# Kernel optimization log

Hardware: AMD Instinct MI355X
Metric: run time of the kernel (lower is better)

Reference implementation:

```python
import jax, jax.numpy as jnp
import numpy as np

L = 48.0      # cubic box edge
DL = 4.0      # k-grid spacing param -> nk = int(L/DL) = 12
N = 8192      # atoms
D = 128       # feature channels
TWOPI = 2.0 * np.pi


def _k_index_sets():
    """Replicates torch mask.nonzero() ordering and the (k_vectors - 1) index
    shift of compute_potential_optimized. The shifted indices are remapped to
    effective integer exponents (torch negative indexing wraps, i.e. modulo)."""
    nk = int(L / DL)
    kx = np.arange(nk + 1)
    ky = np.arange(-nk, nk + 1)
    kz = np.arange(-nk, nk + 1)
    KX, KY, KZ = np.meshgrid(kx, ky, kz, indexing='ij')
    ksq = KX.astype(np.float64) ** 2 + KY ** 2 + KZ ** 2
    mask = (ksq <= (L / DL) ** 2) & (ksq > 0)
    ix, iy, iz = np.nonzero(mask)  # row-major, same order as torch .nonzero()
    # forward potential: value[:, :, ix-1, iy-1, iz-1] with wraparound ->
    # effective exponents via modulo of the per-axis table sizes
    ex = (ix - 1) % (nk + 1)                      # eikx col c -> exponent c
    ey = ((iy - 1) % (2 * nk + 1)) - nk           # eiky col c -> exponent c-nk
    ez = ((iz - 1) % (2 * nk + 1)) - nk
    k_fwd = np.stack([ex, ey, ez], axis=1).astype(np.int32)
    # inverse transform: unshifted valid k-vectors, negative sign in exponent
    k_inv = np.stack([ix, iy - nk, iz - nk], axis=1).astype(np.int32)
    return k_fwd, k_inv


def setup_inputs() -> dict:
    key = jax.random.key(0)
    kq, kk, kv, kr = jax.random.split(key, 4)
    k_fwd, k_inv = _k_index_sets()
    cell = jnp.eye(3, dtype=jnp.float32)[None] * jnp.float32(L)  # [1,3,3]
    return {
        'q_vector': jax.random.normal(kq, (N, D), dtype=jnp.float32),
        'k_vector': jax.random.normal(kk, (N, D), dtype=jnp.float32),
        'v_vector': jax.random.normal(kv, (N, D), dtype=jnp.float32),
        'positions': jax.random.uniform(kr, (N, 3), dtype=jnp.float32) * jnp.float32(L),
        'cell': cell,
        'batch': jnp.zeros((N,), dtype=jnp.int64),
        'k_fwd': jnp.asarray(k_fwd),
        'k_inv': jnp.asarray(k_inv),
    }


def reference(q_vector, k_vector, v_vector, positions, cell, batch, k_fwd, k_inv):
    # single batch (batch is all zeros); box = diagonal of the cell
    box = jnp.diagonal(cell.reshape(-1, 3, 3), axis1=-2, axis2=-1)[0]  # [3]
    rfrac = positions / box                                            # [n,3]
    # plane waves at the selected k-vectors; |eik| == 1
    phase_f = TWOPI * (rfrac @ k_fwd.T.astype(rfrac.dtype))            # [n,K]
    eik_f = jnp.exp(1j * phase_f)                                      # complex64
    phase_i = TWOPI * (rfrac @ k_inv.T.astype(rfrac.dtype))
    eik_i = jnp.exp(-1j * phase_i)                                     # [n,K]
    cdt = eik_f.dtype
    # k/v potentials: structure-factor sums over atoms -> [K,d]
    k_pot = jnp.einsum('nk,nd->kd', eik_f, k_vector.astype(cdt))
    v_pot = jnp.einsum('nk,nd->kd', eik_f, v_vector.astype(cdt))
    # |q_pot[n,d,k]| = |q[n,d]|*|eik[n,k]| = |q[n,d]| exactly, so the einsum
    # 'ijk,jk->ij' over abs values collapses to a real GEMM:
    aw = jnp.abs(q_vector) @ jnp.abs(k_pot).T                          # [n,K]
    # max-shift + log_softmax + exp == softmax over the k axis
    sm = jax.nn.softmax(aw, axis=-1)
    # inverse transform fused: sum_k sm[n,k]*eik_i[n,k]*v_pot[k,d]
    out = jnp.real(jnp.einsum('nk,kd->nd', sm.astype(cdt) * eik_i, v_pot))
    return out
```

## Files before the change

### kernel.cpp

```cpp
#include <hip/hip_runtime.h>
#include <hip/hip_bf16.h>

#define D128 128
#define NSPLIT 4
#define KT 32
#define SNR 32
#define SKT 128
#define TOPS 8
#define FCAP 16

typedef float4 f4;
typedef __attribute__((ext_vector_type(8))) short short8v;
typedef __attribute__((ext_vector_type(4))) float f32x4;

__device__ __forceinline__ unsigned short f2bu(float x){
  __hip_bfloat16 h = __float2bfloat16(x);
  return *(unsigned short*)&h;
}
__device__ __forceinline__ float bu2f(unsigned short u){
  return __uint_as_float(((unsigned)u) << 16);
}

#define GLDS16(gp, lp) __builtin_amdgcn_global_load_lds( \
    (const __attribute__((address_space(1))) unsigned int*)(const void*)(gp), \
    (__attribute__((address_space(3))) unsigned int*)(lp), 16, 0, 0)

__global__ __launch_bounds__(256) void k_prep(const float* __restrict__ pos,
    const float* __restrict__ cell, float* __restrict__ rfrac, int N){
  int i = blockIdx.x*256 + threadIdx.x;
  if(i >= N) return;
  float bx = cell[0], by = cell[4], bz = cell[8];
  f4 r; r.x = pos[i*3+0]/bx; r.y = pos[i*3+1]/by; r.z = pos[i*3+2]/bz; r.w = 0.f;
  ((f4*)rfrac)[i] = r;
}

__global__ __launch_bounds__(256) void k_zero(float* __restrict__ p, int total){
  int i = blockIdx.x*256 + threadIdx.x;
  int stride = gridDim.x*256;
  for(; i < total; i += stride) p[i] = 0.f;
}

__global__ __launch_bounds__(256) void k_cvt(const float* __restrict__ q,
    const float* __restrict__ kvec, const float* __restrict__ vvec,
    unsigned short* __restrict__ kvhT, unsigned short* __restrict__ kvlT,
    unsigned short* __restrict__ vvhT, unsigned short* __restrict__ qa_bf, int N){
  __shared__ float sk[32][132], sv[32][132];
  const int tid = threadIdx.x;
  const int c0 = blockIdx.x*32;
  #pragma unroll
  for(int i=0;i<2;i++){
    int idx = tid + i*256;
    int row = idx >> 4, c = idx & 15;
    const float* src = q + (size_t)(c0+row)*D128 + c*8;
    f4 v0 = *(const f4*)src, v1 = *(const f4*)(src+4);
    uint4 o;
    o.x = (unsigned)f2bu(fabsf(v0.x)) | ((unsigned)f2bu(fabsf(v0.y))<<16);
    o.y = (unsigned)f2bu(fabsf(v0.z)) | ((unsigned)f2bu(fabsf(v0.w))<<16);
    o.z = (unsigned)f2bu(fabsf(v1.x)) | ((unsigned)f2bu(fabsf(v1.y))<<16);
    o.w = (unsigned)f2bu(fabsf(v1.z)) | ((unsigned)f2bu(fabsf(v1.w))<<16);
    *(uint4*)(qa_bf + (size_t)(c0+row)*D128 + ((c ^ (row&7))<<3)) = o;
  }
  #pragma unroll
  for(int i=0;i<4;i++){
    int idx = tid + i*256;
    int a = idx >> 5, fq = idx & 31;
    f4 v = ((const f4*)(kvec + (size_t)(c0+a)*D128))[fq];
    *(f4*)&sk[a][fq*4] = v;
    f4 u = ((const f4*)(vvec + (size_t)(c0+a)*D128))[fq];
    *(f4*)&sv[a][fq*4] = u;
  }
  __syncthreads();
  #pragma unroll
  for(int i=0;i<4;i++){
    int idx = tid + i*256;
    int d = idx >> 3, aq = idx & 7;
    size_t ob = (size_t)d*N + c0 + aq*4;
    ushort4 h, l, vh;
    float x0 = sk[aq*4+0][d], x1 = sk[aq*4+1][d], x2 = sk[aq*4+2][d], x3 = sk[aq*4+3][d];
    h.x = f2bu(x0); h.y = f2bu(x1); h.z = f2bu(x2); h.w = f2bu(x3);
    l.x = f2bu(x0 - bu2f(h.x)); l.y = f2bu(x1 - bu2f(h.y));
    l.z = f2bu(x2 - bu2f(h.z)); l.w = f2bu(x3 - bu2f(h.w));
    vh.x = f2bu(sv[aq*4+0][d]); vh.y = f2bu(sv[aq*4+1][d]);
    vh.z = f2bu(sv[aq*4+2][d]); vh.w = f2bu(sv[aq*4+3][d]);
    *(ushort4*)(kvhT + ob) = h;
    *(ushort4*)(kvlT + ob) = l;
    *(ushort4*)(vvhT + ob) = vh;
  }
}

__global__ __launch_bounds__(512) void k_pot_mfma(
    const unsigned short* __restrict__ kvhT, const unsigned short* __restrict__ kvlT,
    const unsigned short* __restrict__ vvhT, const float* __restrict__ rfrac,
    const int* __restrict__ kfwd, float* __restrict__ pot4, int N, int K){
  const int tid = threadIdx.x;
  const int k0 = blockIdx.x*KT;
  const int split = blockIdx.y;
  const int part = N/NSPLIT;
  const int abase = split*part;
  __shared__ unsigned short Ae[2][4][KT][32];
  __shared__ unsigned short Bl[2][3][D128][32];
  const int w = tid >> 6, l = tid & 63, l15 = l & 15, g = l >> 4;
  const int a = tid & 31, rq = tid >> 5;
  float kfr[2][3];
  {
    int r0 = min(k0 + rq*2,     K-1);
    int r1 = min(k0 + rq*2 + 1, K-1);
    kfr[0][0] = (float)kfwd[3*r0]; kfr[0][1] = (float)kfwd[3*r0+1]; kfr[0][2] = (float)kfwd[3*r0+2];
    kfr[1][0] = (float)kfwd[3*r1]; kfr[1][1] = (float)kfwd[3*r1+1]; kfr[1][2] = (float)kfwd[3*r1+2];
  }
  f32x4 acc[2][4];
  #pragma unroll
  for(int i=0;i<2;i++)
    #pragma unroll
    for(int j=0;j<4;j++)
      acc[i][j] = (f32x4){0.f,0.f,0.f,0.f};
  const int rowS = w*16 + (l >> 2);
  const int csrc = (((l & 3) ^ ((l >> 3) & 3)))*8;
  const int cA   = (g ^ ((l15 >> 1) & 3))*8;

  auto stage = [&](int buf, int c0a){
    size_t goff = (size_t)rowS*N + c0a + csrc;
    GLDS16(kvhT + goff, &Bl[buf][0][w*16][0]);
    GLDS16(kvlT + goff, &Bl[buf][1][w*16][0]);
    GLDS16(vvhT + goff, &Bl[buf][2][w*16][0]);
  };
  auto egen = [&](int buf, int c0a){
    f4 rf = ((const f4*)rfrac)[c0a + a];
    #pragma unroll
    for(int rr=0; rr<2; rr++){
      int r = rq*2 + rr;
      float t = rf.x*kfr[rr][0] + rf.y*kfr[rr][1] + rf.z*kfr[rr][2];
      t -= floorf(t);
      float cv = cospif(2.0f*t), sv = sinpif(2.0f*t);
      unsigned short chb = f2bu(cv);
      unsigned short clb = f2bu(cv - bu2f(chb));
      unsigned short shb = f2bu(sv);
      unsigned short slb = f2bu(sv - bu2f(shb));
      int cp = (((a>>3) ^ ((r>>1)&3)) << 3) | (a & 7);
      Ae[buf][0][r][cp] = chb; Ae[buf][1][r][cp] = clb;
      Ae[buf][2][r][cp] = shb; Ae[buf][3][r][cp] = slb;
    }
  };

  stage(0, abase); egen(0, abase);
  __syncthreads();
  const int nch = part/32;
  for(int ch=0; ch<nch; ch++){
    int cur = ch & 1;
    if(ch+1 < nch){ stage(cur^1, abase + (ch+1)*32); egen(cur^1, abase + (ch+1)*32); }
    short8v eA[2][4];
    #pragma unroll
    for(int ks=0; ks<2; ks++)
      #pragma unroll
      for(int ar=0; ar<4; ar++)
        eA[ks][ar] = *(const short8v*)&Ae[cur][ar][ks*16 + l15][cA];
    short8v bKh = *(const short8v*)&Bl[cur][0][w*16 + l15][cA];
    short8v bKl = *(const short8v*)&Bl[cur][1][w*16 + l15][cA];
    short8v bVh = *(const short8v*)&Bl[cur][2][w*16 + l15][cA];
    #pragma unroll
    for(int ks=0; ks<2; ks++){
      acc[ks][0] = __builtin_amdgcn_mfma_f32_16x16x32_bf16(eA[ks][0], bKh, acc[ks][0], 0,0,0);
      acc[ks][1] = __builtin_amdgcn_mfma_f32_16x16x32_bf16(eA[ks][2], bKh, acc[ks][1], 0,0,0);
      acc[ks][2] = __builtin_amdgcn_mfma_f32_16x16x32_bf16(eA[ks][0], bVh, acc[ks][2], 0,0,0);
      acc[ks][3] = __builtin_amdgcn_mfma_f32_16x16x32_bf16(eA[ks][2], bVh, acc[ks][3], 0,0,0);
      acc[ks][0] = __builtin_amdgcn_mfma_f32_16x16x32_bf16(eA[ks][0], bKl, acc[ks][0], 0,0,0);
      acc[ks][1] = __builtin_amdgcn_mfma_f32_16x16x32_bf16(eA[ks][2], bKl, acc[ks][1], 0,0,0);
      acc[ks][0] = __builtin_amdgcn_mfma_f32_16x16x32_bf16(eA[ks][1], bKh, acc[ks][0], 0,0,0);
      acc[ks][1] = __builtin_amdgcn_mfma_f32_16x16x32_bf16(eA[ks][3], bKh, acc[ks][1], 0,0,0);
    }
    __syncthreads();
  }
  size_t M = (size_t)K*D128;
  #pragma unroll
  for(int ks=0; ks<2; ks++){
    #pragma unroll
    for(int reg=0; reg<4; reg++){
      int k = k0 + ks*16 + g*4 + reg;
      if(k < K){
        int d = w*16 + l15;
        size_t base = (size_t)k*D128 + d;
        atomicAdd(&pot4[base],       acc[ks][0][reg]);
        atomicAdd(&pot4[base + M],   acc[ks][1][reg]);
        atomicAdd(&pot4[base + 2*M], acc[ks][2][reg]);
        atomicAdd(&pot4[base + 3*M], acc[ks][3][reg]);
      }
    }
  }
}

__global__ __launch_bounds__(256) void k_merge(const float* __restrict__ pot4,
    float* __restrict__ kabs, unsigned short* __restrict__ kabs_swz,
    float* __restrict__ vcm, float* __restrict__ vsm, int K, int KPAD){
  size_t M = (size_t)K*D128;
  size_t idx = (size_t)blockIdx.x*256 + threadIdx.x;
  if(idx >= (size_t)KPAD*D128) return;
  int k = (int)(idx >> 7), d = (int)(idx & 127);
  size_t sw = (size_t)k*D128 + ((((d>>3) ^ (k&7))<<3) | (d&7));
  if(idx < M){
    float kc = pot4[idx], ks_ = pot4[M+idx], vc = pot4[2*M+idx], vs = pot4[3*M+idx];
    float ab = sqrtf(fmaf(kc,kc, ks_*ks_));
    kabs[idx] = ab;
    vcm[idx] = vc; vsm[idx] = vs;
    kabs_swz[sw] = f2bu(ab);
  } else {
    kabs_swz[sw] = 0;
  }
}

__global__ __launch_bounds__(256) void k_screen(
    const unsigned short* __restrict__ qa_bf, const unsigned short* __restrict__ kabs_swz,
    int* __restrict__ tk, float* __restrict__ taw, int N, int K, int NT){
  const int tid = threadIdx.x;
  const int w = tid >> 6, l = tid & 63, l15 = l & 15, g = l >> 4;
  const int n0 = blockIdx.x*SNR;
  const int ty = blockIdx.y;
  const int k0 = ty*SKT;
  __shared__ unsigned short Kb[SKT][D128];
  __shared__ unsigned short Qa[SNR][D128];
  __shared__ int cnt[SNR];
  __shared__ unsigned mx[SNR];
  if(tid < SNR){ cnt[tid] = 0; mx[tid] = 0u; }
  {
    int row = tid >> 3, s = tid & 7;
    size_t o = ((size_t)(n0+row)*NT + ty)*TOPS + s;
    taw[o] = -1e30f; tk[o] = -1;
  }
  #pragma unroll
  for(int j=0;j<8;j++){
    int sbase = w*512 + j*64;
    GLDS16(kabs_swz + (size_t)k0*D128 + (size_t)(sbase + l)*8,
           ((unsigned short*)Kb) + (size_t)sbase*8);
  }
  #pragma unroll
  for(int j=0;j<2;j++){
    int sbase = w*128 + j*64;
    GLDS16(qa_bf + (size_t)n0*D128 + (size_t)(sbase + l)*8,
           ((unsigned short*)Qa) + (size_t)sbase*8);
  }
  __syncthreads();
  f32x4 acc[2][2];
  #pragma unroll
  for(int i=0;i<2;i++)
    #pragma unroll
    for(int j=0;j<2;j++)
      acc[i][j] = (f32x4){0.f,0.f,0.f,0.f};
  const int sz = l15 & 7;
  #pragma unroll
  for(int ds=0; ds<4; ds++){
    int c = (((ds*4 + g) ^ sz))*8;
    short8v a0 = *(const short8v*)&Kb[w*32 + l15][c];
    short8v a1 = *(const short8v*)&Kb[w*32 + 16 + l15][c];
    short8v b0 = *(const short8v*)&Qa[l15][c];
    short8v b1 = *(const short8v*)&Qa[16 + l15][c];
    acc[0][0] = __builtin_amdgcn_mfma_f32_16x16x32_bf16(a0, b0, acc[0][0], 0,0,0);
    acc[0][1] = __builtin_amdgcn_mfma_f32_16x16x32_bf16(a0, b1, acc[0][1], 0,0,0);
    acc[1][0] = __builtin_amdgcn_mfma_f32_16x16x32_bf16(a1, b0, acc[1][0], 0,0,0);
    acc[1][1] = __builtin_amdgcn_mfma_f32_16x16x32_bf16(a1, b1, acc[1][1], 0,0,0);
  }
  #pragma unroll
  for(int jn=0; jn<2; jn++){
    float m4 = 0.f;
    #pragma unroll
    for(int ks=0; ks<2; ks++)
      #pragma unroll
      for(int r=0; r<4; r++)
        m4 = fmaxf(m4, acc[ks][jn][r]);
    atomicMax(&mx[jn*16 + l15], __float_as_uint(m4));
  }
  __syncthreads();
  #pragma unroll
  for(int jn=0; jn<2; jn++){
    int n = jn*16 + l15;
    float thr = __uint_as_float(mx[n]) - 21.0f;
    #pragma unroll
    for(int ks=0; ks<2; ks++){
      #pragma unroll
      for(int r=0; r<4; r++){
        int k = k0 + w*32 + ks*16 + g*4 + r;
        float aw = acc[ks][jn][r];
        if(k < K && aw >= thr){
          int s = atomicAdd(&cnt[n], 1);
          if(s < TOPS){
            size_t o = ((size_t)(n0+n)*NT + ty)*TOPS + s;
            taw[o] = aw; tk[o] = k;
          }
        }
      }
    }
  }
}

__global__ __launch_bounds__(256) void k_final(const float* __restrict__ q,
    const float* __restrict__ kabs, const float* __restrict__ vcm,
    const float* __restrict__ vsm, const float* __restrict__ rfrac,
    const int* __restrict__ kinv, const int* __restrict__ tk,
    const float* __restrict__ taw, float* __restrict__ out, int N, int K, int NT){
  const int rb = threadIdx.x >> 2;
  const int j  = threadIdx.x & 3;
  const int row = blockIdx.x*64 + rb;
  if(row >= N) return;
  const int NE = NT*TOPS;
  const float* trow = taw + (size_t)row*NE;
  const int*   krow = tk  + (size_t)row*NE;
  float m = -1e30f;
  for(int i=j; i<NE; i+=4) m = fmaxf(m, trow[i]);
  m = fmaxf(m, __shfl_xor(m,1)); m = fmaxf(m, __shfl_xor(m,2));
  __shared__ int lk[64][FCAP];
  __shared__ int lcnt[64];
  if(j==0) lcnt[rb] = 0;
  __syncthreads();
  for(int i=j; i<NE; i+=4){
    float aw = trow[i];
    if(aw >= m - 24.0f){
      int s = atomicAdd(&lcnt[rb], 1);
      if(s < FCAP) lk[rb][s] = krow[i];
    }
  }
  __syncthreads();
  int cn = min(lcnt[rb], FCAP);
  const float* qrow = q + (size_t)row*D128;
  float paw[FCAP];
  for(int e=0; e<cn; e++){
    int k = lk[rb][e];
    const float* ar = kabs + (size_t)k*D128;
    float p = 0.f;
    #pragma unroll
    for(int d=0; d<32; d+=4){
      int dd = j*32 + d;
      f4 qv = *(const f4*)(qrow+dd); f4 av = *(const f4*)(ar+dd);
      p = fmaf(fabsf(qv.x), av.x, p); p = fmaf(fabsf(qv.y), av.y, p);
      p = fmaf(fabsf(qv.z), av.z, p); p = fmaf(fabsf(qv.w), av.w, p);
    }
    p += __shfl_xor(p,1); p += __shfl_xor(p,2);
    paw[e] = p;
  }
  float m2 = -1e30f;
  for(int e=0;e<cn;e++) m2 = fmaxf(m2, paw[e]);
  float w[FCAP]; float Z = 0.f;
  for(int e=0;e<cn;e++){ w[e] = expf(paw[e]-m2); Z += w[e]; }
  float o[32];
  #pragma unroll
  for(int t=0;t<32;t++) o[t]=0.f;
  f4 rf = *(const f4*)(rfrac + (size_t)row*4);
  for(int e=0;e<cn;e++){
    float wn = w[e]/Z;
    if(wn < 1e-7f) continue;
    int k = lk[rb][e];
    float t = rf.x*(float)kinv[k*3] + rf.y*(float)kinv[k*3+1] + rf.z*(float)kinv[k*3+2];
    t -= floorf(t);
    float si = sinpif(2.0f*t), ci = cospif(2.0f*t);
    float wc = wn*ci, wsn = wn*si;
    const float* vcr = vcm + (size_t)k*D128 + j*32;
    const float* vsr = vsm + (size_t)k*D128 + j*32;
    #pragma unroll
    for(int d=0; d<32; d+=4){
      f4 a2 = *(const f4*)(vcr+d); f4 b2 = *(const f4*)(vsr+d);
      o[d]   = fmaf(wc, a2.x, fmaf(wsn, b2.x, o[d]));
      o[d+1] = fmaf(wc, a2.y, fmaf(wsn, b2.y, o[d+1]));
      o[d+2] = fmaf(wc, a2.z, fmaf(wsn, b2.z, o[d+2]));
      o[d+3] = fmaf(wc, a2.w, fmaf(wsn, b2.w, o[d+3]));
    }
  }
  float* orow = out + (size_t)row*D128 + j*32;
  #pragma unroll
  for(int d=0; d<32; d+=4)
    *(f4*)(orow+d) = make_float4(o[d], o[d+1], o[d+2], o[d+3]);
}

extern "C" void kernel_launch(void* const* d_in, const int* in_sizes, int n_in,
                              void* d_out, int out_size, void* d_ws, size_t ws_size,
                              hipStream_t stream){
  const float* q    = (const float*)d_in[0];
  const float* kvec = (const float*)d_in[1];
  const float* vvec = (const float*)d_in[2];
  const float* pos  = (const float*)d_in[3];
  const float* cell = (const float*)d_in[4];
  const int*   kfwd = (const int*)d_in[6];
  const int*   kinv = (const int*)d_in[7];
  const int N = in_sizes[3]/3;
  const int K = in_sizes[6]/3;
  const int NT = (K + SKT - 1)/SKT;
  const int KPAD = NT*SKT;
  const int KTILES = (K + KT - 1)/KT;

  float* ws = (float*)d_ws;
  size_t o = 0;
  float* rfrac    = ws + o; o += (size_t)N*4;
  float* pot4     = ws + o; o += (size_t)4*K*D128;
  float* kabs     = ws + o; o += (size_t)K*D128;
  float* vcm      = ws + o; o += (size_t)K*D128;
  float* vsm      = ws + o; o += (size_t)K*D128;
  unsigned short* kabs_swz = (unsigned short*)(ws + o); o += (size_t)KPAD*D128/2 + 4;
  unsigned short* qa_bf    = (unsigned short*)(ws + o); o += (size_t)N*D128/2 + 4;
  float* taw      = ws + o; o += (size_t)N*NT*TOPS;
  int*   tk       = (int*)(ws + o); o += (size_t)N*NT*TOPS;
  unsigned short* kvhT = (unsigned short*)(ws + o); o += (size_t)D128*N/2;
  unsigned short* kvlT = (unsigned short*)(ws + o); o += (size_t)D128*N/2;
  unsigned short* vvhT = (unsigned short*)(ws + o); o += (size_t)D128*N/2;
  float* out = (float*)d_out;

  k_prep<<<dim3((N+255)/256), dim3(256), 0, stream>>>(pos, cell, rfrac, N);
  k_zero<<<dim3(1024), dim3(256), 0, stream>>>(pot4, 4*K*D128);
  k_cvt<<<dim3(N/32), dim3(256), 0, stream>>>(q, kvec, vvec, kvhT, kvlT, vvhT, qa_bf, N);
  k_pot_mfma<<<dim3(KTILES, NSPLIT), dim3(512), 0, stream>>>(
      kvhT, kvlT, vvhT, rfrac, kfwd, pot4, N, K);
  k_merge<<<dim3((KPAD*D128 + 255)/256), dim3(256), 0, stream>>>(
      pot4, kabs, kabs_swz, vcm, vsm, K, KPAD);
  k_screen<<<dim3(N/SNR, NT), dim3(256), 0, stream>>>(qa_bf, kabs_swz, tk, taw, N, K, NT);
  k_final<<<dim3((N+63)/64), dim3(256), 0, stream>>>(
      q, kabs, vcm, vsm, rfrac, kinv, tk, taw, out, N, K, NT);
}
```

Baseline: 271.8 us.

## Retile potential MFMA kernel, fuse prep into convert, use hardware sin/cos

The potential kernel now covers 64 k-vectors per block instead of 32 and splits atoms eight ways instead of four. Each thread generates plane-wave values for two atoms and two k-vectors, writing packed 32-bit bf16 pairs to LDS, so each staged B tile is reused across more k rows. The separate position-normalisation kernel is folded into the convert kernel, removing one launch. The sincospi calls are replaced by the hardware fract, sin and cos intrinsics in both the generation and final kernels. That trades accuracy for speed and uses more accumulator registers, which could lower occupancy.

```diff
diff --git a/kernel.cpp b/kernel.cpp
--- a/kernel.cpp
+++ b/kernel.cpp
@@ -2,8 +2,8 @@
 #include <hip/hip_bf16.h>
 
 #define D128 128
-#define NSPLIT 4
-#define KT 32
+#define NSPLIT 8
+#define KT 64
 #define SNR 32
 #define SKT 128
 #define TOPS 8
@@ -25,28 +25,27 @@
     (const __attribute__((address_space(1))) unsigned int*)(const void*)(gp), \
     (__attribute__((address_space(3))) unsigned int*)(lp), 16, 0, 0)
 
-__global__ __launch_bounds__(256) void k_prep(const float* __restrict__ pos,
-    const float* __restrict__ cell, float* __restrict__ rfrac, int N){
-  int i = blockIdx.x*256 + threadIdx.x;
-  if(i >= N) return;
-  float bx = cell[0], by = cell[4], bz = cell[8];
-  f4 r; r.x = pos[i*3+0]/bx; r.y = pos[i*3+1]/by; r.z = pos[i*3+2]/bz; r.w = 0.f;
-  ((f4*)rfrac)[i] = r;
-}
-
 __global__ __launch_bounds__(256) void k_zero(float* __restrict__ p, int total){
   int i = blockIdx.x*256 + threadIdx.x;
   int stride = gridDim.x*256;
   for(; i < total; i += stride) p[i] = 0.f;
 }
 
-__global__ __launch_bounds__(256) void k_cvt(const float* __restrict__ q,
-    const float* __restrict__ kvec, const float* __restrict__ vvec,
-    unsigned short* __restrict__ kvhT, unsigned short* __restrict__ kvlT,
-    unsigned short* __restrict__ vvhT, unsigned short* __restrict__ qa_bf, int N){
+__global__ __launch_bounds__(256) void k_cvt(const float* __restrict__ pos,
+    const float* __restrict__ cell, float* __restrict__ rfrac,
+    const float* __restrict__ q, const float* __restrict__ kvec,
+    const float* __restrict__ vvec, unsigned short* __restrict__ kvhT,
+    unsigned short* __restrict__ kvlT, unsigned short* __restrict__ vvhT,
+    unsigned short* __restrict__ qa_bf, int N){
   __shared__ float sk[32][132], sv[32][132];
   const int tid = threadIdx.x;
   const int c0 = blockIdx.x*32;
+  if(tid < 32){
+    int i = c0 + tid;
+    float bx = cell[0], by = cell[4], bz = cell[8];
+    f4 r; r.x = pos[i*3+0]/bx; r.y = pos[i*3+1]/by; r.z = pos[i*3+2]/bz; r.w = 0.f;
+    ((f4*)rfrac)[i] = r;
+  }
   #pragma unroll
   for(int i=0;i<2;i++){
     int idx = tid + i*256;
@@ -100,17 +99,18 @@
   __shared__ unsigned short Ae[2][4][KT][32];
   __shared__ unsigned short Bl[2][3][D128][32];
   const int w = tid >> 6, l = tid & 63, l15 = l & 15, g = l >> 4;
-  const int a = tid & 31, rq = tid >> 5;
-  float kfr[2][3];
+  const int kp = tid >> 4;
+  const int a0 = (tid & 15)*2;
+  float kfa[2][3];
   {
-    int r0 = min(k0 + rq*2,     K-1);
-    int r1 = min(k0 + rq*2 + 1, K-1);
-    kfr[0][0] = (float)kfwd[3*r0]; kfr[0][1] = (float)kfwd[3*r0+1]; kfr[0][2] = (float)kfwd[3*r0+2];
-    kfr[1][0] = (float)kfwd[3*r1]; kfr[1][1] = (float)kfwd[3*r1+1]; kfr[1][2] = (float)kfwd[3*r1+2];
-  }
-  f32x4 acc[2][4];
-  #pragma unroll
-  for(int i=0;i<2;i++)
+    int r0 = min(k0 + kp*2,     K-1);
+    int r1 = min(k0 + kp*2 + 1, K-1);
+    kfa[0][0] = (float)kfwd[3*r0]; kfa[0][1] = (float)kfwd[3*r0+1]; kfa[0][2] = (float)kfwd[3*r0+2];
+    kfa[1][0] = (float)kfwd[3*r1]; kfa[1][1] = (float)kfwd[3*r1+1]; kfa[1][2] = (float)kfwd[3*r1+2];
+  }
+  f32x4 acc[4][4];
+  #pragma unroll
+  for(int i=0;i<4;i++)
     #pragma unroll
     for(int j=0;j<4;j++)
       acc[i][j] = (f32x4){0.f,0.f,0.f,0.f};
@@ -125,20 +125,30 @@
     GLDS16(vvhT + goff, &Bl[buf][2][w*16][0]);
   };
   auto egen = [&](int buf, int c0a){
-    f4 rf = ((const f4*)rfrac)[c0a + a];
-    #pragma unroll
-    for(int rr=0; rr<2; rr++){
-      int r = rq*2 + rr;
-      float t = rf.x*kfr[rr][0] + rf.y*kfr[rr][1] + rf.z*kfr[rr][2];
-      t -= floorf(t);
-      float cv = cospif(2.0f*t), sv = sinpif(2.0f*t);
-      unsigned short chb = f2bu(cv);
-      unsigned short clb = f2bu(cv - bu2f(chb));
-      unsigned short shb = f2bu(sv);
-      unsigned short slb = f2bu(sv - bu2f(shb));
-      int cp = (((a>>3) ^ ((r>>1)&3)) << 3) | (a & 7);
-      Ae[buf][0][r][cp] = chb; Ae[buf][1][r][cp] = clb;
-      Ae[buf][2][r][cp] = shb; Ae[buf][3][r][cp] = slb;
+    f4 r0 = ((const f4*)rfrac)[c0a + a0];
+    f4 r1 = ((const f4*)rfrac)[c0a + a0 + 1];
+    #pragma unroll
+    for(int kk=0; kk<2; kk++){
+      int kloc = kp*2 + kk;
+      float t0 = __builtin_amdgcn_fractf(r0.x*kfa[kk][0] + r0.y*kfa[kk][1] + r0.z*kfa[kk][2]);
+      float t1 = __builtin_amdgcn_fractf(r1.x*kfa[kk][0] + r1.y*kfa[kk][1] + r1.z*kfa[kk][2]);
+      float c0v = __builtin_amdgcn_cosf(t0), s0v = __builtin_amdgcn_sinf(t0);
+      float c1v = __builtin_amdgcn_cosf(t1), s1v = __builtin_amdgcn_sinf(t1);
+      unsigned cb0 = __float_as_uint(c0v), cb1 = __float_as_uint(c1v);
+      unsigned sb0 = __float_as_uint(s0v), sb1 = __float_as_uint(s1v);
+      unsigned chp = (cb0 >> 16) | (cb1 & 0xffff0000u);
+      unsigned shp = (sb0 >> 16) | (sb1 & 0xffff0000u);
+      float cl0 = c0v - __uint_as_float(cb0 & 0xffff0000u);
+      float cl1 = c1v - __uint_as_float(cb1 & 0xffff0000u);
+      float sl0 = s0v - __uint_as_float(sb0 & 0xffff0000u);
+      float sl1 = s1v - __uint_as_float(sb1 & 0xffff0000u);
+      unsigned clp = (unsigned)f2bu(cl0) | ((unsigned)f2bu(cl1) << 16);
+      unsigned slp = (unsigned)f2bu(sl0) | ((unsigned)f2bu(sl1) << 16);
+      int off = (((a0>>3) ^ ((kloc>>1)&3)) << 3) | (a0 & 7);
+      *(unsigned*)&Ae[buf][0][kloc][off] = chp;
+      *(unsigned*)&Ae[buf][1][kloc][off] = clp;
+      *(unsigned*)&Ae[buf][2][kloc][off] = shp;
+      *(unsigned*)&Ae[buf][3][kloc][off] = slp;
     }
   };
 
@@ -148,31 +158,29 @@
   for(int ch=0; ch<nch; ch++){
     int cur = ch & 1;
     if(ch+1 < nch){ stage(cur^1, abase + (ch+1)*32); egen(cur^1, abase + (ch+1)*32); }
-    short8v eA[2][4];
-    #pragma unroll
-    for(int ks=0; ks<2; ks++)
-      #pragma unroll
-      for(int ar=0; ar<4; ar++)
-        eA[ks][ar] = *(const short8v*)&Ae[cur][ar][ks*16 + l15][cA];
     short8v bKh = *(const short8v*)&Bl[cur][0][w*16 + l15][cA];
     short8v bKl = *(const short8v*)&Bl[cur][1][w*16 + l15][cA];
     short8v bVh = *(const short8v*)&Bl[cur][2][w*16 + l15][cA];
     #pragma unroll
-    for(int ks=0; ks<2; ks++){
-      acc[ks][0] = __builtin_amdgcn_mfma_f32_16x16x32_bf16(eA[ks][0], bKh, acc[ks][0], 0,0,0);
-      acc[ks][1] = __builtin_amdgcn_mfma_f32_16x16x32_bf16(eA[ks][2], bKh, acc[ks][1], 0,0,0);
-      acc[ks][2] = __builtin_amdgcn_mfma_f32_16x16x32_bf16(eA[ks][0], bVh, acc[ks][2], 0,0,0);
-      acc[ks][3] = __builtin_amdgcn_mfma_f32_16x16x32_bf16(eA[ks][2], bVh, acc[ks][3], 0,0,0);
-      acc[ks][0] = __builtin_amdgcn_mfma_f32_16x16x32_bf16(eA[ks][0], bKl, acc[ks][0], 0,0,0);
-      acc[ks][1] = __builtin_amdgcn_mfma_f32_16x16x32_bf16(eA[ks][2], bKl, acc[ks][1], 0,0,0);
-      acc[ks][0] = __builtin_amdgcn_mfma_f32_16x16x32_bf16(eA[ks][1], bKh, acc[ks][0], 0,0,0);
-      acc[ks][1] = __builtin_amdgcn_mfma_f32_16x16x32_bf16(eA[ks][3], bKh, acc[ks][1], 0,0,0);
+    for(int ks=0; ks<4; ks++){
+      short8v e0 = *(const short8v*)&Ae[cur][0][ks*16 + l15][cA];
+      short8v e1 = *(const short8v*)&Ae[cur][1][ks*16 + l15][cA];
+      short8v e2 = *(const short8v*)&Ae[cur][2][ks*16 + l15][cA];
+      short8v e3 = *(const short8v*)&Ae[cur][3][ks*16 + l15][cA];
+      acc[ks][0] = __builtin_amdgcn_mfma_f32_16x16x32_bf16(e0, bKh, acc[ks][0], 0,0,0);
+      acc[ks][1] = __builtin_amdgcn_mfma_f32_16x16x32_bf16(e2, bKh, acc[ks][1], 0,0,0);
+      acc[ks][2] = __builtin_amdgcn_mfma_f32_16x16x32_bf16(e0, bVh, acc[ks][2], 0,0,0);
+      acc[ks][3] = __builtin_amdgcn_mfma_f32_16x16x32_bf16(e2, bVh, acc[ks][3], 0,0,0);
+      acc[ks][0] = __builtin_amdgcn_mfma_f32_16x16x32_bf16(e0, bKl, acc[ks][0], 0,0,0);
+      acc[ks][1] = __builtin_amdgcn_mfma_f32_16x16x32_bf16(e2, bKl, acc[ks][1], 0,0,0);
+      acc[ks][0] = __builtin_amdgcn_mfma_f32_16x16x32_bf16(e1, bKh, acc[ks][0], 0,0,0);
+      acc[ks][1] = __builtin_amdgcn_mfma_f32_16x16x32_bf16(e3, bKh, acc[ks][1], 0,0,0);
     }
     __syncthreads();
   }
   size_t M = (size_t)K*D128;
   #pragma unroll
-  for(int ks=0; ks<2; ks++){
+  for(int ks=0; ks<4; ks++){
     #pragma unroll
     for(int reg=0; reg<4; reg++){
       int k = k0 + ks*16 + g*4 + reg;
@@ -346,9 +354,8 @@
     float wn = w[e]/Z;
     if(wn < 1e-7f) continue;
     int k = lk[rb][e];
-    float t = rf.x*(float)kinv[k*3] + rf.y*(float)kinv[k*3+1] + rf.z*(float)kinv[k*3+2];
-    t -= floorf(t);
-    float si = sinpif(2.0f*t), ci = cospif(2.0f*t);
+    float t = __builtin_amdgcn_fractf(rf.x*(float)kinv[k*3] + rf.y*(float)kinv[k*3+1] + rf.z*(float)kinv[k*3+2]);
+    float si = __builtin_amdgcn_sinf(t), ci = __builtin_amdgcn_cosf(t);
     float wc = wn*ci, wsn = wn*si;
     const float* vcr = vcm + (size_t)k*D128 + j*32;
     const float* vsr = vsm + (size_t)k*D128 + j*32;
@@ -399,9 +406,9 @@
   unsigned short* vvhT = (unsigned short*)(ws + o); o += (size_t)D128*N/2;
   float* out = (float*)d_out;
 
-  k_prep<<<dim3((N+255)/256), dim3(256), 0, stream>>>(pos, cell, rfrac, N);
   k_zero<<<dim3(1024), dim3(256), 0, stream>>>(pot4, 4*K*D128);
-  k_cvt<<<dim3(N/32), dim3(256), 0, stream>>>(q, kvec, vvec, kvhT, kvlT, vvhT, qa_bf, N);
+  k_cvt<<<dim3(N/32), dim3(256), 0, stream>>>(pos, cell, rfrac, q, kvec, vvec,
+      kvhT, kvlT, vvhT, qa_bf, N);
   k_pot_mfma<<<dim3(KTILES, NSPLIT), dim3(512), 0, stream>>>(
       kvhT, kvlT, vvhT, rfrac, kfwd, pot4, N, K);
   k_merge<<<dim3((KPAD*D128 + 255)/256), dim3(256), 0, stream>>>(
```

New measurement: 244.8 us. -9.9%, faster.
